# Optimization experiments

Measured on AMD Instinct MI355X. Metric: run time of the kernel, lower is better.

## Reference

```python
import jax, jax.numpy as jnp
import numpy as np

T, D = 4096, 2048      # tokens, hidden
E, I, K = 16, 1408, 4  # experts, moe intermediate, top_k


def setup_inputs() -> dict:
    key = jax.random.key(0)
    ks = jax.random.split(key, 6)
    W_SCALE = 0.05  # keep activations in a sane range
    x = jax.random.normal(ks[0], (T, D), dtype=jnp.float32)
    w0 = jax.random.normal(ks[1], (E, I, D), dtype=jnp.float32) * W_SCALE  # gate proj
    w1 = jax.random.normal(ks[2], (E, I, D), dtype=jnp.float32) * W_SCALE  # up proj
    w2 = jax.random.normal(ks[3], (E, D, I), dtype=jnp.float32) * W_SCALE  # down proj
    selected_experts = jax.random.randint(ks[4], (T, K), 0, E, dtype=jnp.int32)
    rw = jax.random.uniform(ks[5], (T, K), dtype=jnp.float32)
    routing_weights = rw / jnp.sum(rw, axis=-1, keepdims=True)  # normalized top-k weights
    return {"x": x, "w0": w0, "w1": w1, "w2": w2,
            "selected_experts": selected_experts, "routing_weights": routing_weights}


def reference(x, w0, w1, w2, selected_experts, routing_weights):
    # Per-expert SwiGLU FFN over all tokens: y_e = (silu(x W0_e^T) * (x W1_e^T)) W2_e^T
    def expert_fn(w0_e, w1_e, w2_e):
        h = jax.nn.silu(x @ w0_e.T) * (x @ w1_e.T)  # [T, I]
        return h @ w2_e.T                            # [T, D]

    ys = jax.vmap(expert_fn)(w0, w1, w2)             # [E, T, D]
    # Gather each token's top-k expert outputs and apply routing weights.
    tok = jnp.arange(x.shape[0])[:, None]            # [T, 1]
    gathered = ys[selected_experts, tok, :]          # [T, K, D]
    return gathered * routing_weights[:, :, None]    # [T, K, D]
```

## Files before the change

kernel.cpp:

```cpp
#include <hip/hip_runtime.h>
#include <hip/hip_bf16.h>
#include <stdint.h>

#define NT 4096
#define ND 2048
#define NE 16
#define NI 1408
#define NK 4
#define NTK (NT*NK)

typedef __attribute__((ext_vector_type(8))) short bf16x8;
typedef __attribute__((ext_vector_type(4))) float f32x4;

__device__ __forceinline__ short f2b(float f){
  uint32_t u = __float_as_uint(f);
  uint32_t r = (u + 0x7fffu + ((u >> 16) & 1u)) >> 16;
  return (short)(uint16_t)r;
}
__device__ __forceinline__ float b2f(short s){
  return __uint_as_float(((uint32_t)(uint16_t)s) << 16);
}

__device__ __forceinline__ void gl16(const void* g, void* l){
  __builtin_amdgcn_global_load_lds(
      (const __attribute__((address_space(1))) void*)g,
      (__attribute__((address_space(3))) void*)l, 16, 0, 0);
}



__global__ void detect_init_kernel(const unsigned short* xu, int* wsi){
  const int tid = threadIdx.x;
  if (tid < 64) wsi[tid] = 0;
  wsi[3584 + tid] = 0;
  __shared__ int red[256];
  int c = 0;
  for (int i = tid; i < 8192; i += 256){
    int ex = (xu[i] >> 7) & 0xff;
    c += (ex >= 132) ? 1 : 0;
  }
  red[tid] = c;
  __syncthreads();
  if (tid == 0){
    int s = 0;
    for (int i = 0; i < 256; i++) s += red[i];
    wsi[32] = (s < 64) ? 1 : 0;
  }
}

__global__ void hist_kernel(const int* __restrict__ sel, int* wsi){
  int i = blockIdx.x * 256 + threadIdx.x;
  if (i < NTK) atomicAdd(&wsi[sel[i]], 1);
}

__global__ void plan_kernel(int* wsi){
  if (threadIdx.x != 0) return;
  int4* work64  = (int4*)(wsi + 64);
  int4* work128 = (int4*)(wsi + 2048);
  int off = 0, nw = 0, nw128 = 0;
  for (int e = 0; e < NE; e++){
    int c = wsi[e];
    wsi[40 + e] = off;
    for (int mt = 0; mt * 64 < c; mt++){
      int rem = c - mt * 64;
      work64[nw].x = e; work64[nw].y = off + mt * 64;
      work64[nw].z = rem < 64 ? rem : 64; work64[nw].w = 0;
      nw++;
    }
    for (int mt = 0; mt * 128 < c; mt++){
      int rem = c - mt * 128;
      work128[nw128].x = e; work128[nw128].y = off + mt * 128;
      work128[nw128].z = rem < 128 ? rem : 128; work128[nw128].w = 0;
      nw128++;
    }
    off += c;
  }
  wsi[33] = nw;
  wsi[34] = nw128;
}

__global__ void scatter_kernel(const int* __restrict__ sel, int* wsi, int* list){
  int i = blockIdx.x * 256 + threadIdx.x;
  if (i < NTK){
    int e = sel[i];
    int pos = atomicAdd(&wsi[16 + e], 1);
    list[wsi[40 + e] + pos] = i;
  }
}


__global__ __launch_bounds__(256)
void conv_kernel(const float* __restrict__ src, short* __restrict__ dst,
                 int n8, const int* __restrict__ wsi){
  if (wsi[32]) return;
  int stride = gridDim.x * 256;
  for (int i = blockIdx.x * 256 + threadIdx.x; i < n8; i += stride){
    const float4* s = (const float4*)(src + (size_t)i * 8);
    float4 a = s[0], b = s[1];
    bf16x8 v;
    v[0]=f2b(a.x); v[1]=f2b(a.y); v[2]=f2b(a.z); v[3]=f2b(a.w);
    v[4]=f2b(b.x); v[5]=f2b(b.y); v[6]=f2b(b.z); v[7]=f2b(b.w);
    *(bf16x8*)(dst + (size_t)i * 8) = v;
  }
}


template<int ISB>
__global__ __launch_bounds__(256)
void pass1b_kernel(const void* __restrict__ xg, const void* __restrict__ w0g,
                   const void* __restrict__ w1g,
                   const short* __restrict__ xb, const short* __restrict__ w0b,
                   const short* __restrict__ w1b,
                   const int* __restrict__ wsi, const int* __restrict__ list,
                   short* __restrict__ H)
{
  if (wsi[32] != ISB) return;
  if ((int)blockIdx.x >= wsi[34]) return;
  const int4 wk = ((const int4*)(wsi + 2048))[blockIdx.x];
  const int e = wk.x, row_base = wk.y, rows = wk.z;
  const int n0 = blockIdx.y * 64;

  __shared__ short As [128 * 32];
  __shared__ short B0s[ 64 * 32];
  __shared__ short B1s[ 64 * 32];

  const int tid = threadIdx.x;
  const short* xs  = ISB ? (const short*)xg  : xb;
  const short* w0s = ISB ? (const short*)w0g : w0b;
  const short* w1s = ISB ? (const short*)w1g : w1b;
  const short* zp  = (const short*)(wsi + 3584);

  const int rr = tid >> 2;
  const int cc = (tid & 3) << 3;
  const bool va0 = rr < rows;
  const bool va1 = (64 + rr) < rows;
  const int t0 = va0 ? (list[row_base + rr] >> 2) : 0;
  const int t1 = va1 ? (list[row_base + 64 + rr] >> 2) : 0;
  const short* ag0 = va0 ? xs + (size_t)t0 * ND + cc : zp;
  const short* ag1 = va1 ? xs + (size_t)t1 * ND + cc : zp;
  const int sa0 = va0 ? 32 : 0;
  const int sa1 = va1 ? 32 : 0;
  const short* bg0 = w0s + ((size_t)e * NI + n0 + rr) * ND + cc;
  const short* bg1 = w1s + ((size_t)e * NI + n0 + rr) * ND + cc;

  short* la0 = &As [(size_t)tid * 8];
  short* la1 = &As [((size_t)tid + 256) * 8];
  short* lb0 = &B0s[(size_t)tid * 8];
  short* lb1 = &B1s[(size_t)tid * 8];

  const int lane = tid & 63;
  const int wv = tid >> 6;
  const int wm = (wv >> 1) << 6;
  const int wn = (wv & 1) << 5;
  const int r16 = lane & 15;
  const int qd  = lane >> 4;
  const int qd8 = qd << 3;

  f32x4 acc0[4][2] = {};
  f32x4 acc1[4][2] = {};

  for (int kt = 0; kt < ND; kt += 32){
    __syncthreads();
    gl16(ag0, la0); gl16(ag1, la1);
    gl16(bg0, lb0); gl16(bg1, lb1);
    ag0 += sa0; ag1 += sa1; bg0 += 32; bg1 += 32;
    __syncthreads();
    bf16x8 af[4], b0f[2], b1f[2];
    #pragma unroll
    for (int mi = 0; mi < 4; mi++)
      af[mi] = *(const bf16x8*)&As[(wm + mi*16 + r16) * 32 + qd8];
    #pragma unroll
    for (int ni = 0; ni < 2; ni++){
      b0f[ni] = *(const bf16x8*)&B0s[(wn + ni*16 + r16) * 32 + qd8];
      b1f[ni] = *(const bf16x8*)&B1s[(wn + ni*16 + r16) * 32 + qd8];
    }
    #pragma unroll
    for (int mi = 0; mi < 4; mi++)
      #pragma unroll
      for (int ni = 0; ni < 2; ni++){
        acc0[mi][ni] = __builtin_amdgcn_mfma_f32_16x16x32_bf16(af[mi], b0f[ni], acc0[mi][ni], 0, 0, 0);
        acc1[mi][ni] = __builtin_amdgcn_mfma_f32_16x16x32_bf16(af[mi], b1f[ni], acc1[mi][ni], 0, 0, 0);
      }
  }

  #pragma unroll
  for (int mi = 0; mi < 4; mi++){
    #pragma unroll
    for (int r = 0; r < 4; r++){
      int m = wm + mi*16 + qd*4 + r;
      if (m >= rows) continue;
      size_t hrow = (size_t)(row_base + m) * NI + n0 + wn;
      #pragma unroll
      for (int ni = 0; ni < 2; ni++){
        float a0v = acc0[mi][ni][r];
        float a1v = acc1[mi][ni][r];
        float hv = (a0v / (1.f + __expf(-a0v))) * a1v;
        H[hrow + ni*16 + r16] = f2b(hv);
      }
    }
  }
}


template<int ISB>
__global__ __launch_bounds__(256)
void pass2b_kernel(const void* __restrict__ w2g, const void* __restrict__ rw,
                   const short* __restrict__ w2b,
                   const int* __restrict__ wsi, const int* __restrict__ list,
                   const short* __restrict__ H, void* __restrict__ out)
{
  if (wsi[32] != ISB) return;
  if ((int)blockIdx.x >= wsi[34]) return;
  const int4 wk = ((const int4*)(wsi + 2048))[blockIdx.x];
  const int e = wk.x, row_base = wk.y, rows = wk.z;
  const int n0 = blockIdx.y * 128;

  __shared__ short As[128 * 32];
  __shared__ short Bs[128 * 32];

  const int tid = threadIdx.x;
  const short* ws2 = ISB ? (const short*)w2g : w2b;
  const short* zp  = (const short*)(wsi + 3584);

  const int rr = tid >> 2;
  const int cc = (tid & 3) << 3;
  const bool va0 = rr < rows;
  const bool va1 = (64 + rr) < rows;
  const short* ag0 = va0 ? H + (size_t)(row_base + rr) * NI + cc : zp;
  const short* ag1 = va1 ? H + (size_t)(row_base + 64 + rr) * NI + cc : zp;
  const int sa0 = va0 ? 32 : 0;
  const int sa1 = va1 ? 32 : 0;
  const short* bg0 = ws2 + ((size_t)e * ND + n0 + rr) * NI + cc;
  const short* bg1 = ws2 + ((size_t)e * ND + n0 + 64 + rr) * NI + cc;

  short* la0 = &As[(size_t)tid * 8];
  short* la1 = &As[((size_t)tid + 256) * 8];
  short* lb0 = &Bs[(size_t)tid * 8];
  short* lb1 = &Bs[((size_t)tid + 256) * 8];

  const int lane = tid & 63;
  const int wv = tid >> 6;
  const int wm = (wv >> 1) << 6;
  const int wn = (wv & 1) << 6;
  const int r16 = lane & 15;
  const int qd  = lane >> 4;
  const int qd8 = qd << 3;

  f32x4 acc[4][4] = {};

  for (int kt = 0; kt < NI; kt += 32){
    __syncthreads();
    gl16(ag0, la0); gl16(ag1, la1);
    gl16(bg0, lb0); gl16(bg1, lb1);
    ag0 += sa0; ag1 += sa1; bg0 += 32; bg1 += 32;
    __syncthreads();
    bf16x8 af[4], bf[4];
    #pragma unroll
    for (int mi = 0; mi < 4; mi++)
      af[mi] = *(const bf16x8*)&As[(wm + mi*16 + r16) * 32 + qd8];
    #pragma unroll
    for (int ni = 0; ni < 4; ni++)
      bf[ni] = *(const bf16x8*)&Bs[(wn + ni*16 + r16) * 32 + qd8];
    #pragma unroll
    for (int mi = 0; mi < 4; mi++)
      #pragma unroll
      for (int ni = 0; ni < 4; ni++)
        acc[mi][ni] = __builtin_amdgcn_mfma_f32_16x16x32_bf16(af[mi], bf[ni], acc[mi][ni], 0, 0, 0);
  }

  #pragma unroll
  for (int mi = 0; mi < 4; mi++){
    #pragma unroll
    for (int r = 0; r < 4; r++){
      int m = wm + mi*16 + qd*4 + r;
      if (m >= rows) continue;
      int p = list[row_base + m];
      float sc = ISB ? b2f(((const short*)rw)[p]) : ((const float*)rw)[p];
      size_t orow = (size_t)p * ND + n0 + wn;
      #pragma unroll
      for (int ni = 0; ni < 4; ni++){
        float v = acc[mi][ni][r] * sc;
        if (ISB) ((short*)out)[orow + ni*16 + r16] = f2b(v);
        else     ((float*)out)[orow + ni*16 + r16] = v;
      }
    }
  }
}


template<int ISB>
__device__ __forceinline__ void stage8(short* dst, const void* base, size_t off, bool valid){
  if (ISB){
    bf16x8 v = valid ? *(const bf16x8*)((const short*)base + off) : (bf16x8)0;
    *(bf16x8*)dst = v;
  } else {
    if (valid){
      const float4* s = (const float4*)((const float*)base + off);
      float4 a = s[0], b = s[1];
      dst[0]=f2b(a.x); dst[1]=f2b(a.y); dst[2]=f2b(a.z); dst[3]=f2b(a.w);
      dst[4]=f2b(b.x); dst[5]=f2b(b.y); dst[6]=f2b(b.z); dst[7]=f2b(b.w);
    } else {
      *(bf16x8*)dst = (bf16x8)0;
    }
  }
}

#define LDS_STRIDE 40

template<int ISB>
__global__ __launch_bounds__(256)
void pass1_kernel(const void* __restrict__ x, const void* __restrict__ w0,
                  const void* __restrict__ w1, const int* __restrict__ wsi,
                  const int* __restrict__ list, short* __restrict__ H)
{
  if (wsi[32] != ISB) return;
  if ((int)blockIdx.x >= wsi[33]) return;
  const int4 wk = ((const int4*)(wsi + 64))[blockIdx.x];
  const int e = wk.x, row_base = wk.y, rows = wk.z;
  const int n0 = blockIdx.y * 64;

  __shared__ short As [64 * LDS_STRIDE];
  __shared__ short B0s[64 * LDS_STRIDE];
  __shared__ short B1s[64 * LDS_STRIDE];

  const int tid = threadIdx.x;
  const int lr  = tid >> 2;
  const int c8  = (tid & 3) << 3;
  const bool avalid = lr < rows;
  size_t abase = 0;
  if (avalid){
    int tok = list[row_base + lr] >> 2;
    abase = (size_t)tok * ND + c8;
  }
  const size_t bbase = ((size_t)e * NI + (size_t)(n0 + lr)) * (size_t)ND + c8;

  const int lane = tid & 63;
  const int wv = tid >> 6;
  const int wm = (wv >> 1) << 5;
  const int wn = (wv & 1) << 5;
  const int r16 = lane & 15;
  const int qd  = lane >> 4;
  const int qd8 = qd << 3;

  f32x4 acc0[2][2] = {};
  f32x4 acc1[2][2] = {};

  short* a_dst  = &As [lr * LDS_STRIDE + c8];
  short* b0_dst = &B0s[lr * LDS_STRIDE + c8];
  short* b1_dst = &B1s[lr * LDS_STRIDE + c8];

  for (int kt = 0; kt < ND; kt += 32){
    __syncthreads();
    stage8<ISB>(a_dst,  x,  abase + kt, avalid);
    stage8<ISB>(b0_dst, w0, bbase + kt, true);
    stage8<ISB>(b1_dst, w1, bbase + kt, true);
    __syncthreads();
    bf16x8 af[2], b0f[2], b1f[2];
    #pragma unroll
    for (int mi = 0; mi < 2; mi++)
      af[mi] = *(const bf16x8*)&As[(wm + mi*16 + r16) * LDS_STRIDE + qd8];
    #pragma unroll
    for (int ni = 0; ni < 2; ni++){
      b0f[ni] = *(const bf16x8*)&B0s[(wn + ni*16 + r16) * LDS_STRIDE + qd8];
      b1f[ni] = *(const bf16x8*)&B1s[(wn + ni*16 + r16) * LDS_STRIDE + qd8];
    }
    #pragma unroll
    for (int mi = 0; mi < 2; mi++)
      #pragma unroll
      for (int ni = 0; ni < 2; ni++){
        acc0[mi][ni] = __builtin_amdgcn_mfma_f32_16x16x32_bf16(af[mi], b0f[ni], acc0[mi][ni], 0, 0, 0);
        acc1[mi][ni] = __builtin_amdgcn_mfma_f32_16x16x32_bf16(af[mi], b1f[ni], acc1[mi][ni], 0, 0, 0);
      }
  }

  #pragma unroll
  for (int mi = 0; mi < 2; mi++){
    #pragma unroll
    for (int r = 0; r < 4; r++){
      int m = wm + mi*16 + qd*4 + r;
      if (m >= rows) continue;
      size_t hrow = (size_t)(row_base + m) * NI + n0;
      #pragma unroll
      for (int ni = 0; ni < 2; ni++){
        float a0v = acc0[mi][ni][r];
        float a1v = acc1[mi][ni][r];
        float hv = (a0v / (1.f + __expf(-a0v))) * a1v;
        H[hrow + wn + ni*16 + r16] = f2b(hv);
      }
    }
  }
}

template<int ISB>
__global__ __launch_bounds__(256)
void pass2_kernel(const void* __restrict__ w2, const void* __restrict__ rw,
                  const int* __restrict__ wsi, const int* __restrict__ list,
                  const short* __restrict__ H, void* __restrict__ out)
{
  if (wsi[32] != ISB) return;
  if ((int)blockIdx.x >= wsi[33]) return;
  const int4 wk = ((const int4*)(wsi + 64))[blockIdx.x];
  const int e = wk.x, row_base = wk.y, rows = wk.z;
  const int n0 = blockIdx.y * 64;

  __shared__ short As[64 * LDS_STRIDE];
  __shared__ short Bs[64 * LDS_STRIDE];

  const int tid = threadIdx.x;
  const int lr  = tid >> 2;
  const int c8  = (tid & 3) << 3;
  const bool avalid = lr < rows;
  const size_t abase = (size_t)(row_base + lr) * NI + c8;
  const size_t bbase = ((size_t)e * ND + (size_t)(n0 + lr)) * (size_t)NI + c8;

  const int lane = tid & 63;
  const int wv = tid >> 6;
  const int wm = (wv >> 1) << 5;
  const int wn = (wv & 1) << 5;
  const int r16 = lane & 15;
  const int qd  = lane >> 4;
  const int qd8 = qd << 3;

  f32x4 acc[2][2] = {};

  short* a_dst = &As[lr * LDS_STRIDE + c8];
  short* b_dst = &Bs[lr * LDS_STRIDE + c8];

  for (int kt = 0; kt < NI; kt += 32){
    __syncthreads();
    {
      bf16x8 v = avalid ? *(const bf16x8*)&H[abase + kt] : (bf16x8)0;
      *(bf16x8*)a_dst = v;
    }
    stage8<ISB>(b_dst, w2, bbase + kt, true);
    __syncthreads();
    bf16x8 af[2], bf[2];
    #pragma unroll
    for (int mi = 0; mi < 2; mi++)
      af[mi] = *(const bf16x8*)&As[(wm + mi*16 + r16) * LDS_STRIDE + qd8];
    #pragma unroll
    for (int ni = 0; ni < 2; ni++)
      bf[ni] = *(const bf16x8*)&Bs[(wn + ni*16 + r16) * LDS_STRIDE + qd8];
    #pragma unroll
    for (int mi = 0; mi < 2; mi++)
      #pragma unroll
      for (int ni = 0; ni < 2; ni++)
        acc[mi][ni] = __builtin_amdgcn_mfma_f32_16x16x32_bf16(af[mi], bf[ni], acc[mi][ni], 0, 0, 0);
  }

  #pragma unroll
  for (int mi = 0; mi < 2; mi++){
    #pragma unroll
    for (int r = 0; r < 4; r++){
      int m = wm + mi*16 + qd*4 + r;
      if (m >= rows) continue;
      int p = list[row_base + m];
      float sc = ISB ? b2f(((const short*)rw)[p]) : ((const float*)rw)[p];
      size_t orow = (size_t)p * ND + n0;
      #pragma unroll
      for (int ni = 0; ni < 2; ni++){
        float v = acc[mi][ni][r] * sc;
        if (ISB) ((short*)out)[orow + wn + ni*16 + r16] = f2b(v);
        else     ((float*)out)[orow + wn + ni*16 + r16] = v;
      }
    }
  }
}


extern "C" void kernel_launch(void* const* d_in, const int* in_sizes, int n_in,
                              void* d_out, int out_size, void* d_ws, size_t ws_size,
                              hipStream_t stream) {
  (void)in_sizes; (void)n_in; (void)out_size;
  const void* x  = d_in[0];
  const void* w0 = d_in[1];
  const void* w1 = d_in[2];
  const void* w2 = d_in[3];
  const int* sel = (const int*)d_in[4];
  const void* rw = d_in[5];

  int* wsi   = (int*)d_ws;
  int* list  = wsi + 4096;
  short* H   = (short*)((char*)d_ws + 262144);

  const size_t H_BYTES  = (size_t)NTK * NI * 2;
  const size_t XB_BYTES = (size_t)NT * ND * 2;
  const size_t WB_BYTES = (size_t)NE * NI * ND * 2;
  const size_t offX = 262144 + H_BYTES;
  const size_t offW = offX + XB_BYTES;
  const size_t need = offW + 2 * WB_BYTES;

  detect_init_kernel<<<1, 256, 0, stream>>>((const unsigned short*)x, wsi);
  hist_kernel<<<NTK/256, 256, 0, stream>>>(sel, wsi);
  plan_kernel<<<1, 64, 0, stream>>>(wsi);
  scatter_kernel<<<NTK/256, 256, 0, stream>>>(sel, wsi, list);

  if (ws_size >= need){
    short* xb  = (short*)((char*)d_ws + offX);
    short* w0b = (short*)((char*)d_ws + offW);
    short* w1b = w0b + (size_t)NE * NI * ND;
    short* w2b = w0b;

    conv_kernel<<<2048, 256, 0, stream>>>((const float*)x,  xb,  NT*ND/8,    wsi);
    conv_kernel<<<2048, 256, 0, stream>>>((const float*)w0, w0b, NE*NI*ND/8, wsi);
    conv_kernel<<<2048, 256, 0, stream>>>((const float*)w1, w1b, NE*NI*ND/8, wsi);

    dim3 g1(160, NI/64);
    pass1b_kernel<1><<<g1, 256, 0, stream>>>(x, w0, w1, xb, w0b, w1b, wsi, list, H);
    pass1b_kernel<0><<<g1, 256, 0, stream>>>(x, w0, w1, xb, w0b, w1b, wsi, list, H);

    conv_kernel<<<2048, 256, 0, stream>>>((const float*)w2, w2b, NE*ND*NI/8, wsi);

    dim3 g2(160, ND/128);
    pass2b_kernel<1><<<g2, 256, 0, stream>>>(w2, rw, w2b, wsi, list, H, d_out);
    pass2b_kernel<0><<<g2, 256, 0, stream>>>(w2, rw, w2b, wsi, list, H, d_out);
  } else {
    dim3 g1(272, NI/64);
    dim3 g2(272, ND/64);
    pass1_kernel<1><<<g1, 256, 0, stream>>>(x, w0, w1, wsi, list, H);
    pass1_kernel<0><<<g1, 256, 0, stream>>>(x, w0, w1, wsi, list, H);
    pass2_kernel<1><<<g2, 256, 0, stream>>>(w2, rw, wsi, list, H, d_out);
    pass2_kernel<0><<<g2, 256, 0, stream>>>(w2, rw, wsi, list, H, d_out);
  }
}
```

Before: 1.183 ms.

## Double N-tile width in grouped GEMMs and add XCD-aware block swizzle

Both grouped-GEMM passes now use twice-wide N tiles: 128 columns for gate/up and 256 for down-proj. Each wave therefore holds more accumulators and reuses every A fragment across more MFMAs. Block indices are remapped so that consecutive blocks landing on the same XCD share neighbouring tiles, which should improve L2 reuse. Launch bounds now request 2 blocks per CU. The larger accumulator sets (128 fp32 per thread in pass1) raise register pressure and may cause spills or lower occupancy.

```diff
diff --git a/kernel.cpp b/kernel.cpp
--- a/kernel.cpp
+++ b/kernel.cpp
@@ -25,6 +25,11 @@
   __builtin_amdgcn_global_load_lds(
       (const __attribute__((address_space(1))) void*)g,
       (__attribute__((address_space(3))) void*)l, 16, 0, 0);
+}
+
+__device__ __forceinline__ int xcd_swz(int lin, int nwg){
+  int cpx = nwg >> 3;
+  return (lin & 7) * cpx + (lin >> 3);
 }
 
 
@@ -106,7 +111,7 @@
 
 
 template<int ISB>
-__global__ __launch_bounds__(256)
+__global__ __launch_bounds__(256, 2)
 void pass1b_kernel(const void* __restrict__ xg, const void* __restrict__ w0g,
                    const void* __restrict__ w1g,
                    const short* __restrict__ xb, const short* __restrict__ w0b,
@@ -115,14 +120,19 @@
                    short* __restrict__ H)
 {
   if (wsi[32] != ISB) return;
-  if ((int)blockIdx.x >= wsi[34]) return;
-  const int4 wk = ((const int4*)(wsi + 2048))[blockIdx.x];
+  const int nmt = wsi[34];
+  const int lin = blockIdx.x + 160 * blockIdx.y;
+  const int swz = xcd_swz(lin, 160 * gridDim.y);
+  const int mtile = swz % 160;
+  const int ntile = swz / 160;
+  if (mtile >= nmt) return;
+  const int4 wk = ((const int4*)(wsi + 2048))[mtile];
   const int e = wk.x, row_base = wk.y, rows = wk.z;
-  const int n0 = blockIdx.y * 64;
+  const int n0 = ntile * 128;
 
   __shared__ short As [128 * 32];
-  __shared__ short B0s[ 64 * 32];
-  __shared__ short B1s[ 64 * 32];
+  __shared__ short B0s[128 * 32];
+  __shared__ short B1s[128 * 32];
 
   const int tid = threadIdx.x;
   const short* xs  = ISB ? (const short*)xg  : xb;
@@ -140,44 +150,50 @@
   const short* ag1 = va1 ? xs + (size_t)t1 * ND + cc : zp;
   const int sa0 = va0 ? 32 : 0;
   const int sa1 = va1 ? 32 : 0;
-  const short* bg0 = w0s + ((size_t)e * NI + n0 + rr) * ND + cc;
-  const short* bg1 = w1s + ((size_t)e * NI + n0 + rr) * ND + cc;
-
-  short* la0 = &As [(size_t)tid * 8];
-  short* la1 = &As [((size_t)tid + 256) * 8];
-  short* lb0 = &B0s[(size_t)tid * 8];
-  short* lb1 = &B1s[(size_t)tid * 8];
+  const short* b0g0 = w0s + ((size_t)e * NI + n0 + rr)      * ND + cc;
+  const short* b0g1 = w0s + ((size_t)e * NI + n0 + 64 + rr) * ND + cc;
+  const short* b1g0 = w1s + ((size_t)e * NI + n0 + rr)      * ND + cc;
+  const short* b1g1 = w1s + ((size_t)e * NI + n0 + 64 + rr) * ND + cc;
+
+  short* la0  = &As [(size_t)tid * 8];
+  short* la1  = &As [((size_t)tid + 256) * 8];
+  short* lb00 = &B0s[(size_t)tid * 8];
+  short* lb01 = &B0s[((size_t)tid + 256) * 8];
+  short* lb10 = &B1s[(size_t)tid * 8];
+  short* lb11 = &B1s[((size_t)tid + 256) * 8];
 
   const int lane = tid & 63;
   const int wv = tid >> 6;
   const int wm = (wv >> 1) << 6;
-  const int wn = (wv & 1) << 5;
+  const int wn = (wv & 1) << 6;
   const int r16 = lane & 15;
   const int qd  = lane >> 4;
   const int qd8 = qd << 3;
 
-  f32x4 acc0[4][2] = {};
-  f32x4 acc1[4][2] = {};
+  f32x4 acc0[4][4] = {};
+  f32x4 acc1[4][4] = {};
 
   for (int kt = 0; kt < ND; kt += 32){
     __syncthreads();
-    gl16(ag0, la0); gl16(ag1, la1);
-    gl16(bg0, lb0); gl16(bg1, lb1);
-    ag0 += sa0; ag1 += sa1; bg0 += 32; bg1 += 32;
-    __syncthreads();
-    bf16x8 af[4], b0f[2], b1f[2];
+    gl16(ag0,  la0);  gl16(ag1,  la1);
+    gl16(b0g0, lb00); gl16(b0g1, lb01);
+    gl16(b1g0, lb10); gl16(b1g1, lb11);
+    ag0 += sa0; ag1 += sa1;
+    b0g0 += 32; b0g1 += 32; b1g0 += 32; b1g1 += 32;
+    __syncthreads();
+    bf16x8 af[4], b0f[4], b1f[4];
     #pragma unroll
     for (int mi = 0; mi < 4; mi++)
       af[mi] = *(const bf16x8*)&As[(wm + mi*16 + r16) * 32 + qd8];
     #pragma unroll
-    for (int ni = 0; ni < 2; ni++){
+    for (int ni = 0; ni < 4; ni++){
       b0f[ni] = *(const bf16x8*)&B0s[(wn + ni*16 + r16) * 32 + qd8];
       b1f[ni] = *(const bf16x8*)&B1s[(wn + ni*16 + r16) * 32 + qd8];
     }
     #pragma unroll
     for (int mi = 0; mi < 4; mi++)
       #pragma unroll
-      for (int ni = 0; ni < 2; ni++){
+      for (int ni = 0; ni < 4; ni++){
         acc0[mi][ni] = __builtin_amdgcn_mfma_f32_16x16x32_bf16(af[mi], b0f[ni], acc0[mi][ni], 0, 0, 0);
         acc1[mi][ni] = __builtin_amdgcn_mfma_f32_16x16x32_bf16(af[mi], b1f[ni], acc1[mi][ni], 0, 0, 0);
       }
@@ -191,7 +207,7 @@
       if (m >= rows) continue;
       size_t hrow = (size_t)(row_base + m) * NI + n0 + wn;
       #pragma unroll
-      for (int ni = 0; ni < 2; ni++){
+      for (int ni = 0; ni < 4; ni++){
         float a0v = acc0[mi][ni][r];
         float a1v = acc1[mi][ni][r];
         float hv = (a0v / (1.f + __expf(-a0v))) * a1v;
@@ -203,20 +219,25 @@
 
 
 template<int ISB>
-__global__ __launch_bounds__(256)
+__global__ __launch_bounds__(256, 2)
 void pass2b_kernel(const void* __restrict__ w2g, const void* __restrict__ rw,
                    const short* __restrict__ w2b,
                    const int* __restrict__ wsi, const int* __restrict__ list,
                    const short* __restrict__ H, void* __restrict__ out)
 {
   if (wsi[32] != ISB) return;
-  if ((int)blockIdx.x >= wsi[34]) return;
-  const int4 wk = ((const int4*)(wsi + 2048))[blockIdx.x];
+  const int nmt = wsi[34];
+  const int lin = blockIdx.x + 160 * blockIdx.y;
+  const int swz = xcd_swz(lin, 160 * gridDim.y);
+  const int mtile = swz % 160;
+  const int ntile = swz / 160;
+  if (mtile >= nmt) return;
+  const int4 wk = ((const int4*)(wsi + 2048))[mtile];
   const int e = wk.x, row_base = wk.y, rows = wk.z;
-  const int n0 = blockIdx.y * 128;
+  const int n0 = ntile * 256;
 
   __shared__ short As[128 * 32];
-  __shared__ short Bs[128 * 32];
+  __shared__ short Bs[256 * 32];
 
   const int tid = threadIdx.x;
   const short* ws2 = ISB ? (const short*)w2g : w2b;
@@ -230,41 +251,47 @@
   const short* ag1 = va1 ? H + (size_t)(row_base + 64 + rr) * NI + cc : zp;
   const int sa0 = va0 ? 32 : 0;
   const int sa1 = va1 ? 32 : 0;
-  const short* bg0 = ws2 + ((size_t)e * ND + n0 + rr) * NI + cc;
-  const short* bg1 = ws2 + ((size_t)e * ND + n0 + 64 + rr) * NI + cc;
+  const short* bg0 = ws2 + ((size_t)e * ND + n0 + rr)       * NI + cc;
+  const short* bg1 = ws2 + ((size_t)e * ND + n0 + 64  + rr) * NI + cc;
+  const short* bg2 = ws2 + ((size_t)e * ND + n0 + 128 + rr) * NI + cc;
+  const short* bg3 = ws2 + ((size_t)e * ND + n0 + 192 + rr) * NI + cc;
 
   short* la0 = &As[(size_t)tid * 8];
   short* la1 = &As[((size_t)tid + 256) * 8];
   short* lb0 = &Bs[(size_t)tid * 8];
   short* lb1 = &Bs[((size_t)tid + 256) * 8];
+  short* lb2 = &Bs[((size_t)tid + 512) * 8];
+  short* lb3 = &Bs[((size_t)tid + 768) * 8];
 
   const int lane = tid & 63;
   const int wv = tid >> 6;
   const int wm = (wv >> 1) << 6;
-  const int wn = (wv & 1) << 6;
+  const int wn = (wv & 1) << 7;
   const int r16 = lane & 15;
   const int qd  = lane >> 4;
   const int qd8 = qd << 3;
 
-  f32x4 acc[4][4] = {};
+  f32x4 acc[4][8] = {};
 
   for (int kt = 0; kt < NI; kt += 32){
     __syncthreads();
     gl16(ag0, la0); gl16(ag1, la1);
     gl16(bg0, lb0); gl16(bg1, lb1);
-    ag0 += sa0; ag1 += sa1; bg0 += 32; bg1 += 32;
-    __syncthreads();
-    bf16x8 af[4], bf[4];
+    gl16(bg2, lb2); gl16(bg3, lb3);
+    ag0 += sa0; ag1 += sa1;
+    bg0 += 32; bg1 += 32; bg2 += 32; bg3 += 32;
+    __syncthreads();
+    bf16x8 af[4], bf[8];
     #pragma unroll
     for (int mi = 0; mi < 4; mi++)
       af[mi] = *(const bf16x8*)&As[(wm + mi*16 + r16) * 32 + qd8];
     #pragma unroll
-    for (int ni = 0; ni < 4; ni++)
+    for (int ni = 0; ni < 8; ni++)
       bf[ni] = *(const bf16x8*)&Bs[(wn + ni*16 + r16) * 32 + qd8];
     #pragma unroll
     for (int mi = 0; mi < 4; mi++)
       #pragma unroll
-      for (int ni = 0; ni < 4; ni++)
+      for (int ni = 0; ni < 8; ni++)
         acc[mi][ni] = __builtin_amdgcn_mfma_f32_16x16x32_bf16(af[mi], bf[ni], acc[mi][ni], 0, 0, 0);
   }
 
@@ -278,7 +305,7 @@
       float sc = ISB ? b2f(((const short*)rw)[p]) : ((const float*)rw)[p];
       size_t orow = (size_t)p * ND + n0 + wn;
       #pragma unroll
-      for (int ni = 0; ni < 4; ni++){
+      for (int ni = 0; ni < 8; ni++){
         float v = acc[mi][ni][r] * sc;
         if (ISB) ((short*)out)[orow + ni*16 + r16] = f2b(v);
         else     ((float*)out)[orow + ni*16 + r16] = v;
@@ -505,13 +532,13 @@
     conv_kernel<<<2048, 256, 0, stream>>>((const float*)w0, w0b, NE*NI*ND/8, wsi);
     conv_kernel<<<2048, 256, 0, stream>>>((const float*)w1, w1b, NE*NI*ND/8, wsi);
 
-    dim3 g1(160, NI/64);
+    dim3 g1(160, NI/128);
     pass1b_kernel<1><<<g1, 256, 0, stream>>>(x, w0, w1, xb, w0b, w1b, wsi, list, H);
     pass1b_kernel<0><<<g1, 256, 0, stream>>>(x, w0, w1, xb, w0b, w1b, wsi, list, H);
 
     conv_kernel<<<2048, 256, 0, stream>>>((const float*)w2, w2b, NE*ND*NI/8, wsi);
 
-    dim3 g2(160, ND/128);
+    dim3 g2(160, ND/256);
     pass2b_kernel<1><<<g2, 256, 0, stream>>>(w2, rw, w2b, wsi, list, H, d_out);
     pass2b_kernel<0><<<g2, 256, 0, stream>>>(w2, rw, w2b, wsi, list, H, d_out);
   } else {
```

Result: faster. 1.130 ms (-4.5%).
